# Kernel optimization log

Measured on AMD Instinct MI355X. Metric: run time of the kernel, lower is better.

The kernel has to match this reference:

```python
import jax, jax.numpy as jnp
import numpy as np

TEMPERATURE = 0.2
EPS = 1e-12

def _l2norm(v, axis=-1):
    return v / jnp.maximum(jnp.linalg.norm(v, axis=axis, keepdims=True), EPS)

def setup_inputs() -> dict:
    key = jax.random.key(0)
    k1, k2, k3, k4, k5 = jax.random.split(key, 5)
    B, D, P, K = 4096, 256, 100, 10
    return {
        "x": jax.random.normal(k1, (B, D), dtype=jnp.float32),
        "x_aug": jax.random.normal(k2, (B, D), dtype=jnp.float32),
        "proto_w": jax.random.normal(k3, (P, D), dtype=jnp.float32),
        "hard_q": jax.random.randint(k4, (2, B), 0, P, dtype=jnp.int32),
        "neg_q": jax.random.randint(k5, (2, B, K), 0, P, dtype=jnp.int32),
    }

def reference(x, x_aug, proto_w, hard_q, neg_q):
    # graphcl.loss_cal with args.hard_selection=True, args.proto_dist=True,
    # args.sample_dist=False. The original O(n^2) python loops are vectorized
    # as gathers/broadcasts; math is identical.
    B = x.shape[0]
    P = proto_w.shape[0]
    out1 = _l2norm(x)                      # [B, D]
    out2 = _l2norm(x_aug)                  # [B, D]
    out = jnp.concatenate([out1, out2], 0) # [2B, D]
    n = 2 * B

    sim = jnp.exp(out @ out.T / TEMPERATURE)          # [2B, 2B]
    eye = jnp.eye(n, dtype=bool)

    hq = hard_q.reshape(-1)                # [2B]  (concat of the two views)
    nq = neg_q.reshape(n, -1)              # [2B, K]

    # hard_selection: mask[i,j] = (i != j) and (hard_q[j] in neg_q[i]).
    # Build per-prototype membership [2B, P], then gather columns by hq[j].
    mem_proto = (nq[:, :, None] == jnp.arange(P, dtype=nq.dtype)[None, None, :]).any(1)  # [2B, P]
    member = jnp.take(mem_proto, hq, axis=1)          # [2B, 2B]
    mask = (~eye) & member

    # proto_dist reweighting (prototypes used via .data, i.e. detached).
    w = _l2norm(jax.lax.stop_gradient(proto_w))       # [P, D]
    pd = 1.0 - w @ w.T                                # [P, P]
    rw = jnp.where(eye, 0.0, pd[hq[:, None], hq[None, :]])  # [2B, 2B]
    rmin = rw.min(axis=1, keepdims=True)
    rmax = rw.max(axis=1, keepdims=True)
    rw = (rw - rmin) / (rmax - rmin)
    # NOTE: torch broadcasts (2B,2B) - (2B,) along columns -> mu[None, :]
    mu = rw.mean(axis=1)
    std = jnp.std(rw, axis=1, ddof=1)  # torch.std default: unbiased
    rw = jnp.exp((rw - mu[None, :]) ** 2 / (2.0 * std[None, :] ** 2))
    sim = sim * rw

    pos = jnp.exp(jnp.sum(out1 * out2, axis=-1) / TEMPERATURE)  # [B]
    pos = jnp.concatenate([pos, pos], 0)                        # [2B]
    # masked_select(...).sum(dim=-1) in the original sums ALL kept entries.
    denom = jnp.sum(jnp.where(mask, sim, 0.0))
    loss = jnp.mean(-jnp.log(pos / denom))
    return loss
```

## Files before the change

### kernel.cpp

```cpp
#include <hip/hip_runtime.h>
#include <cmath>

#define BB   4096
#define DD   256
#define NN   8192
#define PP   100
#define KK   10

typedef float f32x16 __attribute__((ext_vector_type(16)));
typedef long  lx2    __attribute__((ext_vector_type(2)));

constexpr size_t OFF_DPART = 0;
constexpr size_t OFF_PPART = 4096;
constexpr size_t OFF_CNT   = 8192;
constexpr size_t OFF_MU    = 8704;
constexpr size_t OFF_SD    = 9216;
constexpr size_t OFF_RWN   = 9728;
constexpr size_t OFF_PI    = 56128;
constexpr size_t OFF_INVP  = 88896;
constexpr size_t OFF_HQP   = 121664;
constexpr size_t OFF_CTABT = 154432;
constexpr size_t OFF_G     = 3431232;


__global__ __launch_bounds__(256) void sortzero_kernel(
    const int* __restrict__ hq, int* __restrict__ cnt,
    int* __restrict__ pi, int* __restrict__ invp, int* __restrict__ hqp,
    double* __restrict__ dpart, double* __restrict__ ppart) {
    const int blk = blockIdx.x;
    const int t = threadIdx.x;
    if (blk == 16) {
        for (int k = t; k < 512; k += 256) { dpart[k] = 0.0; ppart[k] = 0.0; }
        __shared__ int hh[PP];
        if (t < PP) hh[t] = 0;
        __syncthreads();
#pragma unroll
        for (int r = 0; r < 32; ++r) atomicAdd(&hh[hq[r * 256 + t]], 1);
        __syncthreads();
        if (t < PP) cnt[t] = hh[t];
        return;
    }
    __shared__ int h[16][PP];
    __shared__ int tot[PP];
    __shared__ int gbase[PP];
    __shared__ int base[PP];
    int* hf = &h[0][0];
    for (int k = t; k < 16 * PP; k += 256) hf[k] = 0;
    __syncthreads();
#pragma unroll
    for (int r = 0; r < 32; ++r) {
        const int i = r * 256 + t;
        atomicAdd(&h[r >> 1][hq[i]], 1);
    }
    __syncthreads();
    if (t < PP) {
        int pre = 0, s = 0;
#pragma unroll
        for (int ch = 0; ch < 16; ++ch) {
            if (ch == blk) pre = s;
            s += h[ch][t];
        }
        tot[t] = s;
        base[t] = pre;
    }
    __syncthreads();
    if (t == 0) {
        int run = 0;
        for (int c = 0; c < PP; ++c) { gbase[c] = run; run += tot[c]; }
    }
    __syncthreads();
    if (t < PP) base[t] += gbase[t];
    __syncthreads();
#pragma unroll
    for (int r = 0; r < 2; ++r) {
        const int i = blk * 512 + r * 256 + t;
        const int c = hq[i];
        const int d = atomicAdd(&base[c], 1);
        pi[d] = i;
        hqp[d] = c;
        invp[i] = d;
    }
}

__global__ __launch_bounds__(256) void norm_protopd_kernel(
    const float* __restrict__ x, const float* __restrict__ xa,
    const float* __restrict__ pw, const int* __restrict__ invp,
    const int* __restrict__ cnt, char* __restrict__ Gpb, double* __restrict__ ppart,
    float* __restrict__ rwn, float* __restrict__ mu, float* __restrict__ sd) {
    const int blk = blockIdx.x;
    const int t = threadIdx.x;
    if (blk < 256) {
        const int wv = t >> 6, lane = t & 63;
        const int w = blk * 4 + wv;
        float4 v1[4], v2[4];
        int p1[4], p2[4];
#pragma unroll
        for (int s = 0; s < 4; ++s) {
            const int i = w + 1024 * s;
            v1[s] = *(const float4*)(x  + (size_t)i * DD + lane * 4);
            v2[s] = *(const float4*)(xa + (size_t)i * DD + lane * 4);
            p1[s] = invp[i];
            p2[s] = invp[i + BB];
        }
        const int q = lane >> 3, halfsel = (lane >> 1) & 1, pairsel = (lane >> 2) & 1;
        const int bo = pairsel * 8 + 4 * (lane & 1);
        double psum = 0.0;
#pragma unroll
        for (int s = 0; s < 4; ++s) {
            float a = v1[s].x * v1[s].x + v1[s].y * v1[s].y + v1[s].z * v1[s].z + v1[s].w * v1[s].w;
            float b = v2[s].x * v2[s].x + v2[s].y * v2[s].y + v2[s].z * v2[s].z + v2[s].w * v2[s].w;
            float c = v1[s].x * v2[s].x + v1[s].y * v2[s].y + v1[s].z * v2[s].z + v1[s].w * v2[s].w;
#pragma unroll
            for (int off = 32; off > 0; off >>= 1) {
                a += __shfl_xor(a, off);
                b += __shfl_xor(b, off);
                c += __shfl_xor(c, off);
            }
            const float d1 = fmaxf(sqrtf(a), 1e-12f), i1 = 1.0f / d1;
            const float d2 = fmaxf(sqrtf(b), 1e-12f), i2 = 1.0f / d2;
            int w1 = __builtin_amdgcn_cvt_pk_fp8_f32(v1[s].x * i1, v1[s].y * i1, 0, false);
            w1 = __builtin_amdgcn_cvt_pk_fp8_f32(v1[s].z * i1, v1[s].w * i1, w1, true);
            int w2 = __builtin_amdgcn_cvt_pk_fp8_f32(v2[s].x * i2, v2[s].y * i2, 0, false);
            w2 = __builtin_amdgcn_cvt_pk_fp8_f32(v2[s].z * i2, v2[s].w * i2, w2, true);
            const size_t a1 = (size_t)((p1[s] >> 5) * 8192 + q * 1024 +
                                       (halfsel * 32 + (p1[s] & 31)) * 16 + bo);
            const size_t a2 = (size_t)((p2[s] >> 5) * 8192 + q * 1024 +
                                       (halfsel * 32 + (p2[s] & 31)) * 16 + bo);
            *(int*)(Gpb + a1) = w1;
            *(int*)(Gpb + a2) = w2;
            psum += (double)(c * i1 * i2);
        }
        if (lane == 0) atomicAdd(&ppart[w & 511], psum);
    } else {
        const int a = blk - 256;
        __shared__ alignas(16) float wa[DD];
        __shared__ float pdrow[PP];
        __shared__ float r4[4];
        float av = pw[(size_t)a * DD + t];
        float ss = av * av;
#pragma unroll
        for (int off = 32; off > 0; off >>= 1) ss += __shfl_down(ss, off);
        if ((t & 63) == 0) r4[t >> 6] = ss;
        __syncthreads();
        const float na = fmaxf(sqrtf(r4[0] + r4[1] + r4[2] + r4[3]), 1e-12f);
        wa[t] = av / na;
        __syncthreads();
        if (t < PP) {
            const float4* wc = (const float4*)(pw + (size_t)t * DD);
            float dot = 0.f, nb = 0.f;
#pragma unroll 4
            for (int k = 0; k < 64; ++k) {
                const float4 w = wc[k];
                const float4 u = *(const float4*)(wa + 4 * k);
                dot += u.x * w.x + u.y * w.y + u.z * w.z + u.w * w.w;
                nb += w.x * w.x + w.y * w.y + w.z * w.z + w.w * w.w;
            }
            pdrow[t] = 1.0f - dot / fmaxf(sqrtf(nb), 1e-12f);
        }
        __syncthreads();
        if (t < 64) {
            const int lane = t;
            float vmin = 0.f, vmax = 0.f;
            for (int b = lane; b < PP; b += 64) {
                int cc = cnt[b] - (b == a ? 1 : 0);
                if (cc > 0) {
                    float v = pdrow[b];
                    vmin = fminf(vmin, v);
                    vmax = fmaxf(vmax, v);
                }
            }
#pragma unroll
            for (int off = 32; off > 0; off >>= 1) {
                vmin = fminf(vmin, __shfl_xor(vmin, off));
                vmax = fmaxf(vmax, __shfl_xor(vmax, off));
            }
            const float den = vmax - vmin;
            const float inv = (den > 0.f) ? 1.f / den : 0.f;
            double s1 = 0.0, s2 = 0.0;
            for (int b = lane; b < PP; b += 64) {
                float v = (pdrow[b] - vmin) * inv;
                rwn[a * PP + b] = v;
                int cc = cnt[b] - (b == a ? 1 : 0);
                if (cc > 0) { double dv = v; s1 += cc * dv; s2 += cc * dv * dv; }
            }
            if (lane == 0) { double v0 = (0.0 - (double)vmin) * inv; s1 += v0; s2 += v0 * v0; }
#pragma unroll
            for (int off = 32; off > 0; off >>= 1) {
                s1 += __shfl_xor(s1, off);
                s2 += __shfl_xor(s2, off);
            }
            if (lane == 0) {
                double m = s1 / (double)NN;
                double var = (s2 - (double)NN * m * m) / (double)(NN - 1);
                mu[a] = (float)m;
                sd[a] = (float)sqrt(fmax(var, 0.0));
            }
        }
    }
}

__global__ __launch_bounds__(256) void ctab_kernel(
    const int* __restrict__ pi, const int* __restrict__ hqp, const int* __restrict__ nq,
    const float* __restrict__ rwn, const float* __restrict__ mu, const float* __restrict__ sd,
    float* __restrict__ CtabT) {
    const int p0 = blockIdx.x * 32;
    const int t = threadIdx.x;
    __shared__ unsigned long long bits[32][2];
    __shared__ int cls[32];
    __shared__ float smu[PP], ssd[PP];
    if (t < 32) {
        const int p = p0 + t;
        const int* row = nq + (size_t)pi[p] * KK;
        unsigned long long b0 = 0, b1 = 0;
#pragma unroll
        for (int k = 0; k < KK; ++k) {
            int c = row[k];
            if (c < 64) b0 |= 1ull << c; else b1 |= 1ull << (c - 64);
        }
        bits[t][0] = b0;
        bits[t][1] = b1;
        cls[t] = hqp[p];
    }
    if (t < PP) { smu[t] = mu[t]; ssd[t] = sd[t]; }
    __syncthreads();
    for (int idx = t; idx < 32 * PP; idx += 256) {
        const int c = idx >> 5;
        const int pl = idx & 31;
        const bool m = (c < 64) ? ((bits[pl][0] >> c) & 1) : ((bits[pl][1] >> (c - 64)) & 1);
        float v = 0.f;
        if (m) {
            float d = rwn[cls[pl] * PP + c] - smu[c];
            float s = ssd[c];
            v = expf(d * d / (2.0f * s * s));
        }
        CtabT[(size_t)c * NN + p0 + pl] = v;
    }
}

__device__ __forceinline__ void gload_lds16(void* g, void* l) {
    typedef __attribute__((address_space(1))) void* as1_void_p;
    typedef __attribute__((address_space(3))) void* as3_void_p;
    __builtin_amdgcn_global_load_lds((as1_void_p)g, (as3_void_p)l, 16, 0, 0);
}

__global__ __launch_bounds__(256) void sim_kernel(
    const char* __restrict__ Gpb, const int* __restrict__ hqp,
    const float* __restrict__ CtabT, double* __restrict__ dpart) {
    const int xcd = blockIdx.x & 7;
    int idx0 = blockIdx.x >> 3;
    if (idx0 >= 496 + (xcd >> 1) * 16) return;
    int idx = idx0;
    int bj = 0, bi = 0;
#pragma unroll
    for (int q = 0; q < 16; ++q) {
        const int bjq = xcd + 8 * q;
        const int c = (bjq >> 1) + 1;
        if (idx < c) { bj = bjq; bi = idx; break; }
        idx -= c;
    }

    const int t = threadIdx.x;
    const int lane = t & 63;
    const int wv = t >> 6;
    const int i0w = bi * 128 + wv * 32;
    const int j0 = bj * 64;

    __shared__ alignas(16) char lB[16384];

    const char* pa = Gpb + (size_t)(i0w >> 5) * 8192 + lane * 16;
    lx2 a[8];
#pragma unroll
    for (int q = 0; q < 8; ++q) a[q] = *(const lx2*)(pa + q * 1024);

    char* gB = const_cast<char*>(Gpb) + (size_t)(j0 >> 5) * 8192;
#pragma unroll
    for (int s = 0; s < 4; ++s) {
        const int off = (s * 4 + wv) * 1024;
        gload_lds16(gB + off + lane * 16, lB + off);
    }

    const int cl = lane & 31, h = lane >> 5;
    const int col0 = j0 + cl;
    const int col1 = j0 + 32 + cl;
    const int cls0 = hqp[col0];
    const int cls1 = hqp[col1];
    int4 rcg[4];
#pragma unroll
    for (int g = 0; g < 4; ++g)
        rcg[g] = *(const int4*)(hqp + i0w + 8 * g + 4 * h);

    __syncthreads();

    f32x16 acc[2] = {};
#pragma unroll
    for (int q = 0; q < 8; ++q) {
        const lx2 b0 = *(const lx2*)(lB + q * 1024 + lane * 16);
        const lx2 b1 = *(const lx2*)(lB + 8192 + q * 1024 + lane * 16);
        acc[0] = __builtin_amdgcn_mfma_f32_32x32x16_fp8_fp8(a[q].x, b0.x, acc[0], 0, 0, 0);
        acc[1] = __builtin_amdgcn_mfma_f32_32x32x16_fp8_fp8(a[q].x, b1.x, acc[1], 0, 0, 0);
        acc[0] = __builtin_amdgcn_mfma_f32_32x32x16_fp8_fp8(a[q].y, b0.y, acc[0], 0, 0, 0);
        acc[1] = __builtin_amdgcn_mfma_f32_32x32x16_fp8_fp8(a[q].y, b1.y, acc[1], 0, 0, 0);
    }

    const float* ct0 = CtabT + (size_t)cls0 * NN;
    const float* ct1 = CtabT + (size_t)cls1 * NN;
    float4 cf0[4], cf1[4];
    float c20[4][4], c21[4][4];
#pragma unroll
    for (int g = 0; g < 4; ++g) {
        const int rbase = i0w + 8 * g + 4 * h;
        cf0[g] = *(const float4*)(ct0 + rbase);
        cf1[g] = *(const float4*)(ct1 + rbase);
        const int rcv[4] = {rcg[g].x, rcg[g].y, rcg[g].z, rcg[g].w};
#pragma unroll
        for (int r = 0; r < 4; ++r) {
            const float* ctr = CtabT + (size_t)rcv[r] * NN;
            c20[g][r] = ctr[col0];
            c21[g][r] = ctr[col1];
        }
    }
    float partial = 0.f;
#pragma unroll
    for (int g = 0; g < 4; ++g) {
        const int rbase = i0w + 8 * g + 4 * h;
        const float* f0 = (const float*)&cf0[g];
        const float* f1 = (const float*)&cf1[g];
#pragma unroll
        for (int r = 0; r < 4; ++r) {
            const int row = rbase + r;
            const float e0 = __expf(acc[0][4 * g + r] * 5.0f);
            const float e1 = __expf(acc[1][4 * g + r] * 5.0f);
            partial += (row < col0) ? e0 * (f0[r] + c20[g][r]) : 0.f;
            partial += (row < col1) ? e1 * (f1[r] + c21[g][r]) : 0.f;
        }
    }
#pragma unroll
    for (int off = 32; off > 0; off >>= 1) partial += __shfl_down(partial, off);
    __shared__ float wsum[4];
    if (lane == 0) wsum[wv] = partial;
    __syncthreads();
    if (t == 0) {
        const int slot = (xcd * 8 + (idx0 & 7)) * 8 + ((idx0 >> 3) & 7);
        atomicAdd(&dpart[slot], (double)(wsum[0] + wsum[1] + wsum[2] + wsum[3]));
    }
}

__global__ void finalize_kernel(const double* __restrict__ dpart,
                                const double* __restrict__ ppart, float* __restrict__ out) {
    const int lane = threadIdx.x;
    double d = 0.0, p = 0.0;
#pragma unroll
    for (int k = 0; k < 8; ++k) {
        d += dpart[lane + 64 * k];
        p += ppart[lane + 64 * k];
    }
#pragma unroll
    for (int off = 32; off > 0; off >>= 1) {
        d += __shfl_down(d, off);
        p += __shfl_down(p, off);
    }
    if (lane == 0) out[0] = (float)(log(d) - p * (5.0 / 4096.0));
}

extern "C" void kernel_launch(void* const* d_in, const int* in_sizes, int n_in,
                              void* d_out, int out_size, void* d_ws, size_t ws_size,
                              hipStream_t stream) {
    const float* x  = (const float*)d_in[0];
    const float* xa = (const float*)d_in[1];
    const float* pw = (const float*)d_in[2];
    const int* hq   = (const int*)d_in[3];
    const int* nq   = (const int*)d_in[4];
    float* out      = (float*)d_out;

    char* ws = (char*)d_ws;
    double* dpart = (double*)(ws + OFF_DPART);
    double* ppart = (double*)(ws + OFF_PPART);
    int* cnt      = (int*)(ws + OFF_CNT);
    float* mu     = (float*)(ws + OFF_MU);
    float* sd     = (float*)(ws + OFF_SD);
    float* rwn    = (float*)(ws + OFF_RWN);
    int* pi       = (int*)(ws + OFF_PI);
    int* invp     = (int*)(ws + OFF_INVP);
    int* hqp      = (int*)(ws + OFF_HQP);
    float* CtabT  = (float*)(ws + OFF_CTABT);
    char* Gpb     = (char*)(ws + OFF_G);

    sortzero_kernel<<<17, 256, 0, stream>>>(hq, cnt, pi, invp, hqp, dpart, ppart);
    norm_protopd_kernel<<<356, 256, 0, stream>>>(x, xa, pw, invp, cnt, Gpb, ppart,
                                                 rwn, mu, sd);
    ctab_kernel<<<NN / 32, 256, 0, stream>>>(pi, hqp, nq, rwn, mu, sd, CtabT);
    sim_kernel<<<8 * 544, 256, 0, stream>>>(Gpb, hqp, CtabT, dpart);
    finalize_kernel<<<1, 64, 0, stream>>>(dpart, ppart, out);
}
```

Baseline: 123.4 us.

## Pair two column tiles per block in sim kernel to reuse A fragments

Each sim_kernel block now handles two 64-column tiles (bj and bj+8) for the same 128-row stripe, with the first tile skipped when it lies outside the triangle. The A-fragment loads and row-class lookups are shared across both tiles, and the grid shrinks from 544 to 288 blocks per XCD. This cuts redundant global loads of A and per-block launch overhead, at the cost of doubling LDS per block to 32KB and raising register pressure, which may lower occupancy.

```diff
diff --git a/kernel.cpp b/kernel.cpp
--- a/kernel.cpp
+++ b/kernel.cpp
@@ -247,43 +247,59 @@
     const char* __restrict__ Gpb, const int* __restrict__ hqp,
     const float* __restrict__ CtabT, double* __restrict__ dpart) {
     const int xcd = blockIdx.x & 7;
-    int idx0 = blockIdx.x >> 3;
-    if (idx0 >= 496 + (xcd >> 1) * 16) return;
+    const int idx0 = blockIdx.x >> 3;
+    const int nval = 4 * xcd + 264 - 4 * (xcd & 1);
+    if (idx0 >= nval) return;
     int idx = idx0;
-    int bj = 0, bi = 0;
-#pragma unroll
-    for (int q = 0; q < 16; ++q) {
-        const int bjq = xcd + 8 * q;
-        const int c = (bjq >> 1) + 1;
-        if (idx < c) { bj = bjq; bi = idx; break; }
-        idx -= c;
-    }
+    int m = 0, bi = 0;
+#pragma unroll
+    for (int mm = 0; mm < 8; ++mm) {
+        const int cB = ((xcd + 16 * mm) >> 1) + 5;
+        if (idx < cB) { m = mm; bi = idx; break; }
+        idx -= cB;
+    }
+    const int bjA = xcd + 16 * m;
+    const int bjB = bjA + 8;
+    const bool doA = (bi <= (bjA >> 1));
 
     const int t = threadIdx.x;
     const int lane = t & 63;
     const int wv = t >> 6;
     const int i0w = bi * 128 + wv * 32;
-    const int j0 = bj * 64;
-
-    __shared__ alignas(16) char lB[16384];
+    const int j0A = bjA * 64;
+    const int j0B = bjB * 64;
+
+    __shared__ alignas(16) char lB[32768];
 
     const char* pa = Gpb + (size_t)(i0w >> 5) * 8192 + lane * 16;
     lx2 a[8];
 #pragma unroll
     for (int q = 0; q < 8; ++q) a[q] = *(const lx2*)(pa + q * 1024);
 
-    char* gB = const_cast<char*>(Gpb) + (size_t)(j0 >> 5) * 8192;
-#pragma unroll
-    for (int s = 0; s < 4; ++s) {
-        const int off = (s * 4 + wv) * 1024;
-        gload_lds16(gB + off + lane * 16, lB + off);
+    if (doA) {
+        char* gBA = const_cast<char*>(Gpb) + (size_t)bjA * 16384;
+#pragma unroll
+        for (int s = 0; s < 4; ++s) {
+            const int off = (s * 4 + wv) * 1024;
+            gload_lds16(gBA + off + lane * 16, lB + off);
+        }
+    }
+    {
+        char* gBB = const_cast<char*>(Gpb) + (size_t)bjB * 16384;
+#pragma unroll
+        for (int s = 0; s < 4; ++s) {
+            const int off = (s * 4 + wv) * 1024;
+            gload_lds16(gBB + off + lane * 16, lB + 16384 + off);
+        }
     }
 
     const int cl = lane & 31, h = lane >> 5;
-    const int col0 = j0 + cl;
-    const int col1 = j0 + 32 + cl;
-    const int cls0 = hqp[col0];
-    const int cls1 = hqp[col1];
+    const int colA0 = j0A + cl, colA1 = j0A + 32 + cl;
+    const int colB0 = j0B + cl, colB1 = j0B + 32 + cl;
+    const int clsA0 = hqp[colA0];
+    const int clsA1 = hqp[colA1];
+    const int clsB0 = hqp[colB0];
+    const int clsB1 = hqp[colB1];
     int4 rcg[4];
 #pragma unroll
     for (int g = 0; g < 4; ++g)
@@ -291,49 +307,96 @@
 
     __syncthreads();
 
-    f32x16 acc[2] = {};
-#pragma unroll
-    for (int q = 0; q < 8; ++q) {
-        const lx2 b0 = *(const lx2*)(lB + q * 1024 + lane * 16);
-        const lx2 b1 = *(const lx2*)(lB + 8192 + q * 1024 + lane * 16);
-        acc[0] = __builtin_amdgcn_mfma_f32_32x32x16_fp8_fp8(a[q].x, b0.x, acc[0], 0, 0, 0);
-        acc[1] = __builtin_amdgcn_mfma_f32_32x32x16_fp8_fp8(a[q].x, b1.x, acc[1], 0, 0, 0);
-        acc[0] = __builtin_amdgcn_mfma_f32_32x32x16_fp8_fp8(a[q].y, b0.y, acc[0], 0, 0, 0);
-        acc[1] = __builtin_amdgcn_mfma_f32_32x32x16_fp8_fp8(a[q].y, b1.y, acc[1], 0, 0, 0);
-    }
-
-    const float* ct0 = CtabT + (size_t)cls0 * NN;
-    const float* ct1 = CtabT + (size_t)cls1 * NN;
-    float4 cf0[4], cf1[4];
-    float c20[4][4], c21[4][4];
-#pragma unroll
-    for (int g = 0; g < 4; ++g) {
-        const int rbase = i0w + 8 * g + 4 * h;
-        cf0[g] = *(const float4*)(ct0 + rbase);
-        cf1[g] = *(const float4*)(ct1 + rbase);
-        const int rcv[4] = {rcg[g].x, rcg[g].y, rcg[g].z, rcg[g].w};
-#pragma unroll
-        for (int r = 0; r < 4; ++r) {
-            const float* ctr = CtabT + (size_t)rcv[r] * NN;
-            c20[g][r] = ctr[col0];
-            c21[g][r] = ctr[col1];
-        }
-    }
     float partial = 0.f;
-#pragma unroll
-    for (int g = 0; g < 4; ++g) {
-        const int rbase = i0w + 8 * g + 4 * h;
-        const float* f0 = (const float*)&cf0[g];
-        const float* f1 = (const float*)&cf1[g];
-#pragma unroll
-        for (int r = 0; r < 4; ++r) {
-            const int row = rbase + r;
-            const float e0 = __expf(acc[0][4 * g + r] * 5.0f);
-            const float e1 = __expf(acc[1][4 * g + r] * 5.0f);
-            partial += (row < col0) ? e0 * (f0[r] + c20[g][r]) : 0.f;
-            partial += (row < col1) ? e1 * (f1[r] + c21[g][r]) : 0.f;
-        }
-    }
+
+    if (doA) {
+        f32x16 acc[2] = {};
+#pragma unroll
+        for (int q = 0; q < 8; ++q) {
+            const lx2 b0 = *(const lx2*)(lB + q * 1024 + lane * 16);
+            const lx2 b1 = *(const lx2*)(lB + 8192 + q * 1024 + lane * 16);
+            acc[0] = __builtin_amdgcn_mfma_f32_32x32x16_fp8_fp8(a[q].x, b0.x, acc[0], 0, 0, 0);
+            acc[1] = __builtin_amdgcn_mfma_f32_32x32x16_fp8_fp8(a[q].x, b1.x, acc[1], 0, 0, 0);
+            acc[0] = __builtin_amdgcn_mfma_f32_32x32x16_fp8_fp8(a[q].y, b0.y, acc[0], 0, 0, 0);
+            acc[1] = __builtin_amdgcn_mfma_f32_32x32x16_fp8_fp8(a[q].y, b1.y, acc[1], 0, 0, 0);
+        }
+        const float* ct0 = CtabT + (size_t)clsA0 * NN;
+        const float* ct1 = CtabT + (size_t)clsA1 * NN;
+        float4 cf0[4], cf1[4];
+        float c20[4][4], c21[4][4];
+#pragma unroll
+        for (int g = 0; g < 4; ++g) {
+            const int rbase = i0w + 8 * g + 4 * h;
+            cf0[g] = *(const float4*)(ct0 + rbase);
+            cf1[g] = *(const float4*)(ct1 + rbase);
+            const int rcv[4] = {rcg[g].x, rcg[g].y, rcg[g].z, rcg[g].w};
+#pragma unroll
+            for (int r = 0; r < 4; ++r) {
+                const float* ctr = CtabT + (size_t)rcv[r] * NN;
+                c20[g][r] = ctr[colA0];
+                c21[g][r] = ctr[colA1];
+            }
+        }
+#pragma unroll
+        for (int g = 0; g < 4; ++g) {
+            const int rbase = i0w + 8 * g + 4 * h;
+            const float* f0 = (const float*)&cf0[g];
+            const float* f1 = (const float*)&cf1[g];
+#pragma unroll
+            for (int r = 0; r < 4; ++r) {
+                const int row = rbase + r;
+                const float e0 = __expf(acc[0][4 * g + r] * 5.0f);
+                const float e1 = __expf(acc[1][4 * g + r] * 5.0f);
+                partial += (row < colA0) ? e0 * (f0[r] + c20[g][r]) : 0.f;
+                partial += (row < colA1) ? e1 * (f1[r] + c21[g][r]) : 0.f;
+            }
+        }
+    }
+
+    {
+        f32x16 acc[2] = {};
+#pragma unroll
+        for (int q = 0; q < 8; ++q) {
+            const lx2 b0 = *(const lx2*)(lB + 16384 + q * 1024 + lane * 16);
+            const lx2 b1 = *(const lx2*)(lB + 24576 + q * 1024 + lane * 16);
+            acc[0] = __builtin_amdgcn_mfma_f32_32x32x16_fp8_fp8(a[q].x, b0.x, acc[0], 0, 0, 0);
+            acc[1] = __builtin_amdgcn_mfma_f32_32x32x16_fp8_fp8(a[q].x, b1.x, acc[1], 0, 0, 0);
+            acc[0] = __builtin_amdgcn_mfma_f32_32x32x16_fp8_fp8(a[q].y, b0.y, acc[0], 0, 0, 0);
+            acc[1] = __builtin_amdgcn_mfma_f32_32x32x16_fp8_fp8(a[q].y, b1.y, acc[1], 0, 0, 0);
+        }
+        const float* ct0 = CtabT + (size_t)clsB0 * NN;
+        const float* ct1 = CtabT + (size_t)clsB1 * NN;
+        float4 cf0[4], cf1[4];
+        float c20[4][4], c21[4][4];
+#pragma unroll
+        for (int g = 0; g < 4; ++g) {
+            const int rbase = i0w + 8 * g + 4 * h;
+            cf0[g] = *(const float4*)(ct0 + rbase);
+            cf1[g] = *(const float4*)(ct1 + rbase);
+            const int rcv[4] = {rcg[g].x, rcg[g].y, rcg[g].z, rcg[g].w};
+#pragma unroll
+            for (int r = 0; r < 4; ++r) {
+                const float* ctr = CtabT + (size_t)rcv[r] * NN;
+                c20[g][r] = ctr[colB0];
+                c21[g][r] = ctr[colB1];
+            }
+        }
+#pragma unroll
+        for (int g = 0; g < 4; ++g) {
+            const int rbase = i0w + 8 * g + 4 * h;
+            const float* f0 = (const float*)&cf0[g];
+            const float* f1 = (const float*)&cf1[g];
+#pragma unroll
+            for (int r = 0; r < 4; ++r) {
+                const int row = rbase + r;
+                const float e0 = __expf(acc[0][4 * g + r] * 5.0f);
+                const float e1 = __expf(acc[1][4 * g + r] * 5.0f);
+                partial += (row < colB0) ? e0 * (f0[r] + c20[g][r]) : 0.f;
+                partial += (row < colB1) ? e1 * (f1[r] + c21[g][r]) : 0.f;
+            }
+        }
+    }
+
 #pragma unroll
     for (int off = 32; off > 0; off >>= 1) partial += __shfl_down(partial, off);
     __shared__ float wsum[4];
@@ -389,6 +452,6 @@
     norm_protopd_kernel<<<356, 256, 0, stream>>>(x, xa, pw, invp, cnt, Gpb, ppart,
                                                  rwn, mu, sd);
     ctab_kernel<<<NN / 32, 256, 0, stream>>>(pi, hqp, nq, rwn, mu, sd, CtabT);
-    sim_kernel<<<8 * 544, 256, 0, stream>>>(Gpb, hqp, CtabT, dpart);
+    sim_kernel<<<8 * 288, 256, 0, stream>>>(Gpb, hqp, CtabT, dpart);
     finalize_kernel<<<1, 64, 0, stream>>>(dpart, ppart, out);
 }
```

Result: slower. 128.2 us (+3.9%).
